# Performance work log

Measured on AMD Instinct MI355X. Metric: run time of the kernel, lower is better.

The kernel has to match this reference:

```python
import jax, jax.numpy as jnp
import numpy as np

A, C, H, W = 8, 256, 80, 108      # agents, channels, cf_h, cf_w from the module
NUM_CLASSES = 7
OUT_H, OUT_W = 256, 256


def warp_affine(feat, M):
    """Bilinear affine warp of feat [C,H,W] with sampling matrix M [2,3].
    dst(u,v) = src(M @ [u,v,1]); out-of-bounds samples are zero (kornia zero padding)."""
    c, h, w = feat.shape
    vs, us = jnp.meshgrid(jnp.arange(h, dtype=feat.dtype),
                          jnp.arange(w, dtype=feat.dtype), indexing='ij')
    sx = M[0, 0] * us + M[0, 1] * vs + M[0, 2]
    sy = M[1, 0] * us + M[1, 1] * vs + M[1, 2]
    x0 = jnp.floor(sx)
    y0 = jnp.floor(sy)
    wx = sx - x0
    wy = sy - y0
    x0i = x0.astype(jnp.int32)
    y0i = y0.astype(jnp.int32)

    def tap(yy, xx, wgt):
        valid = (yy >= 0) & (yy < h) & (xx >= 0) & (xx < w)
        yyc = jnp.clip(yy, 0, h - 1)
        xxc = jnp.clip(xx, 0, w - 1)
        return feat[:, yyc, xxc] * (wgt * valid)[None]

    return (tap(y0i, x0i, (1 - wy) * (1 - wx))
            + tap(y0i, x0i + 1, (1 - wy) * wx)
            + tap(y0i + 1, x0i, wy * (1 - wx))
            + tap(y0i + 1, x0i + 1, wy * wx))


def resize_bilinear_align_corners(img, oh, ow):
    """F.interpolate(..., mode='bilinear', align_corners=True) for img [N,C,H,W]."""
    h, w = img.shape[-2:]
    ys = jnp.linspace(0.0, h - 1.0, oh, dtype=img.dtype)
    xs = jnp.linspace(0.0, w - 1.0, ow, dtype=img.dtype)
    y0 = jnp.clip(jnp.floor(ys).astype(jnp.int32), 0, h - 2)
    x0 = jnp.clip(jnp.floor(xs).astype(jnp.int32), 0, w - 2)
    wy = (ys - y0)[None, None, :, None]
    wx = (xs - x0)[None, None, None, :]
    row = img[:, :, y0, :] * (1 - wy) + img[:, :, y0 + 1, :] * wy   # [N,C,oh,W]
    return row[:, :, :, x0] * (1 - wx) + row[:, :, :, x0 + 1] * wx  # [N,C,oh,ow]


def setup_inputs() -> dict:
    key = jax.random.key(0)
    k1, k2, k3, k4, k5, k6 = jax.random.split(key, 6)
    x = jax.random.normal(k1, (A, C, H, W), jnp.float32)
    # near-identity per-pair affine sampling matrices with small rotation/shear + translation
    rel = jnp.tile(jnp.eye(2, 3, dtype=jnp.float32), (A, A, 1, 1))
    rel = rel + 0.05 * jax.random.normal(k2, (A, A, 2, 3), jnp.float32)
    rel = rel.at[..., 2].add(10.0 * jax.random.normal(k3, (A, A, 2), jnp.float32))
    adjacency_matrix = jax.random.randint(k4, (A, A), 0, 2, dtype=jnp.int32)
    car_masks = jax.random.uniform(k5, (A, 256, 256), jnp.float32)
    w_cls = 0.02 * jax.random.normal(k6, (NUM_CLASSES, C), jnp.float32)
    b_cls = jnp.zeros((NUM_CLASSES,), jnp.float32)
    return {"x": x, "relative_tfs": rel, "adjacency_matrix": adjacency_matrix,
            "car_masks": car_masks, "w_cls": w_cls, "b_cls": b_cls}


def reference(x, relative_tfs, adjacency_matrix, car_masks, w_cls, b_cls):
    # x = x + F.interpolate(car_masks.unsqueeze(1), (cf_h, cf_w), 'bilinear')  (align_corners=False)
    cm = jax.image.resize(car_masks[:, None], (A, 1, H, W), method="bilinear")
    x = x + cm

    # aggregate_features: per ego-agent i, warp all agents' features into i's frame,
    # zero agents with adjacency[i,j]==0, and sum over j.
    warp_all = jax.vmap(warp_affine)                       # over agents j
    warped = jax.vmap(lambda Ms: warp_all(x, Ms))(relative_tfs)  # [A,A,C,H,W]
    fov = (adjacency_matrix != 0).astype(x.dtype)          # [A,A]
    aggr = jnp.einsum('ij,ijchw->ichw', fov, warped)       # masked sum over j

    def predict(f):  # mask_prediction (1x1 conv) + sigmoid
        logits = jnp.einsum('oc,achw->aohw', w_cls, f) + b_cls[None, :, None, None]
        return jax.nn.sigmoid(logits)

    solo_x = resize_bilinear_align_corners(predict(x), OUT_H, OUT_W)
    aggr_x = resize_bilinear_align_corners(predict(aggr), OUT_H, OUT_W)
    return (solo_x, aggr_x)
```

## Files before the change

### kernel.cpp

```cpp
#include <hip/hip_runtime.h>
#include <hip/hip_bf16.h>

#define A_N 8
#define C_N 256
#define H_N 80
#define W_N 108
#define P_N (H_N * W_N)
#define P4_N (P_N / 4)
#define O_N 7
#define MH 256
#define MW 256
#define OUT_HW 256
#define TPA 34
#define NCG 4

__device__ __forceinline__ float sigmoidf_(float zv) {
    return 1.0f / (1.0f + __expf(-zv));
}

__launch_bounds__(256, 2)
__global__ void k_convp(const float* __restrict__ x, const float* __restrict__ masks,
                        const float* __restrict__ w, float* __restrict__ part)
{
    __shared__ float4 s_red[O_N][NCG][64];
    __shared__ float  s_w[512];
    __shared__ float  s_cm[256];

    const int tid  = threadIdx.x;
    const int lane = tid & 63;
    const int wid  = tid >> 6;
    const int bi   = blockIdx.x;
    const int cg   = bi & 3;
    const int t2   = bi >> 2;
    const int tile = t2 % TPA;
    const int a    = t2 / TPA;

    if (tid < 64) {
        const int c = cg * 64 + tid;
        #pragma unroll
        for (int o = 0; o < 8; ++o)
            s_w[tid * 8 + o] = (o < O_N) ? w[o * C_N + c] : 0.0f;
    }

    {
        const int px = tile * 256 + tid;
        const int pc = min(px, P_N - 1);
        const int oy = pc / W_N, ox = pc - oy * W_N;
        const float ksy = 256.0f / 80.0f;
        const float ksx = 256.0f / 108.0f;
        const float rky = 0.3125f;
        const float rkx = 0.421875f;
        const float sfy = ((float)oy + 0.5f) * ksy - 0.5f;
        const float sfx = ((float)ox + 0.5f) * ksx - 0.5f;
        const int iyS = (int)ceilf(sfy - ksy);
        const int ixS = (int)ceilf(sfx - ksx);

        float wxv[5];
        float wxs = 0.0f;
        #pragma unroll
        for (int q = 0; q < 5; ++q) {
            const int ix = ixS + q;
            float wv = fmaxf(0.0f, 1.0f - fabsf(sfx - (float)ix) * rkx);
            wv = (ix >= 0 && ix < MW) ? wv : 0.0f;
            wxv[q] = wv;
            wxs += wv;
        }
        const float* mp = masks + (size_t)a * (MH * MW);
        float acm = 0.0f, wys = 0.0f;
        #pragma unroll
        for (int r = 0; r < 7; ++r) {
            const int iy = iyS + r;
            float wy = fmaxf(0.0f, 1.0f - fabsf(sfy - (float)iy) * rky);
            wy = (iy >= 0 && iy < MH) ? wy : 0.0f;
            wys += wy;
            const float* row = mp + min(max(iy, 0), MH - 1) * MW;
            float rs = 0.0f;
            #pragma unroll
            for (int q = 0; q < 5; ++q)
                rs = fmaf(wxv[q], row[min(max(ixS + q, 0), MW - 1)], rs);
            acm = fmaf(wy, rs, acm);
        }
        s_cm[tid] = acm / (wys * wxs);
    }
    __syncthreads();

    const int px4  = tile * 64 + lane;
    const int px4c = min(px4, P4_N - 1);
    const float* xp = x + ((size_t)a * C_N + cg * 64 + wid) * P_N + (size_t)px4c * 4;

#define LD(k) const float4 v##k = *reinterpret_cast<const float4*>(xp + (size_t)(4 * (k)) * P_N);
    LD(0)  LD(1)  LD(2)  LD(3)  LD(4)  LD(5)  LD(6)  LD(7)
    LD(8)  LD(9)  LD(10) LD(11) LD(12) LD(13) LD(14) LD(15)
#undef LD

    const float4 cm4 = reinterpret_cast<const float4*>(s_cm)[lane];

    float4 acc[O_N];
    #pragma unroll
    for (int o = 0; o < O_N; ++o) acc[o] = make_float4(0.f, 0.f, 0.f, 0.f);

#define FMA(k)                                                                 \
    {                                                                          \
        float4 v = v##k;                                                       \
        v.x += cm4.x; v.y += cm4.y; v.z += cm4.z; v.w += cm4.w;                \
        const float* wc = s_w + (wid + 4 * (k)) * 8;         \
        const float4 wA = *reinterpret_cast<const float4*>(wc);                \
        const float4 wB = *reinterpret_cast<const float4*>(wc + 4);            \
        acc[0].x = fmaf(wA.x, v.x, acc[0].x); acc[0].y = fmaf(wA.x, v.y, acc[0].y); \
        acc[0].z = fmaf(wA.x, v.z, acc[0].z); acc[0].w = fmaf(wA.x, v.w, acc[0].w); \
        acc[1].x = fmaf(wA.y, v.x, acc[1].x); acc[1].y = fmaf(wA.y, v.y, acc[1].y); \
        acc[1].z = fmaf(wA.y, v.z, acc[1].z); acc[1].w = fmaf(wA.y, v.w, acc[1].w); \
        acc[2].x = fmaf(wA.z, v.x, acc[2].x); acc[2].y = fmaf(wA.z, v.y, acc[2].y); \
        acc[2].z = fmaf(wA.z, v.z, acc[2].z); acc[2].w = fmaf(wA.z, v.w, acc[2].w); \
        acc[3].x = fmaf(wA.w, v.x, acc[3].x); acc[3].y = fmaf(wA.w, v.y, acc[3].y); \
        acc[3].z = fmaf(wA.w, v.z, acc[3].z); acc[3].w = fmaf(wA.w, v.w, acc[3].w); \
        acc[4].x = fmaf(wB.x, v.x, acc[4].x); acc[4].y = fmaf(wB.x, v.y, acc[4].y); \
        acc[4].z = fmaf(wB.x, v.z, acc[4].z); acc[4].w = fmaf(wB.x, v.w, acc[4].w); \
        acc[5].x = fmaf(wB.y, v.x, acc[5].x); acc[5].y = fmaf(wB.y, v.y, acc[5].y); \
        acc[5].z = fmaf(wB.y, v.z, acc[5].z); acc[5].w = fmaf(wB.y, v.w, acc[5].w); \
        acc[6].x = fmaf(wB.z, v.x, acc[6].x); acc[6].y = fmaf(wB.z, v.y, acc[6].y); \
        acc[6].z = fmaf(wB.z, v.z, acc[6].z); acc[6].w = fmaf(wB.z, v.w, acc[6].w); \
    }
    FMA(0)  FMA(1)  FMA(2)  FMA(3)  FMA(4)  FMA(5)  FMA(6)  FMA(7)
    FMA(8)  FMA(9)  FMA(10) FMA(11) FMA(12) FMA(13) FMA(14) FMA(15)
#undef FMA

    #pragma unroll
    for (int o = 0; o < O_N; ++o)
        s_red[o][wid][lane] = acc[o];
    __syncthreads();

    for (int pair = tid; pair < 64 * O_N; pair += 256) {
        const int pl = pair & 63;
        const int o  = pair >> 6;
        const int pg = tile * 64 + pl;
        if (pg >= P4_N) continue;
        const float4 s0 = s_red[o][0][pl];
        const float4 s1 = s_red[o][1][pl];
        const float4 s2 = s_red[o][2][pl];
        const float4 s3 = s_red[o][3][pl];
        float4 pv;
        pv.x = s0.x + s1.x + s2.x + s3.x;
        pv.y = s0.y + s1.y + s2.y + s3.y;
        pv.z = s0.z + s1.z + s2.z + s3.z;
        pv.w = s0.w + s1.w + s2.w + s3.w;
        reinterpret_cast<float4*>(part)[((size_t)(cg * A_N + a) * O_N + o) * P4_N + pg] = pv;
    }
}

__launch_bounds__(256)
__global__ void k_finalize(const float* __restrict__ part, const float* __restrict__ b,
                           float* __restrict__ z, float* __restrict__ ssolo)
{
    const int id = blockIdx.x * 256 + threadIdx.x;
    if (id >= A_N * O_N * P4_N) return;
    const int px4 = id % P4_N;
    const int ao  = id / P4_N;
    const int o   = ao % O_N;

    const float4* p4 = reinterpret_cast<const float4*>(part);
    float4 s = p4[((size_t)(0 * A_N * O_N) + ao) * P4_N + px4];
    #pragma unroll
    for (int g = 1; g < NCG; ++g) {
        const float4 t = p4[((size_t)(g * A_N * O_N) + ao) * P4_N + px4];
        s.x += t.x; s.y += t.y; s.z += t.z; s.w += t.w;
    }
    reinterpret_cast<float4*>(z)[(size_t)ao * P4_N + px4] = s;
    const float bo = b[o];
    float4 sv;
    sv.x = sigmoidf_(s.x + bo);
    sv.y = sigmoidf_(s.y + bo);
    sv.z = sigmoidf_(s.z + bo);
    sv.w = sigmoidf_(s.w + bo);
    reinterpret_cast<float4*>(ssolo)[(size_t)ao * P4_N + px4] = sv;
}

__launch_bounds__(64)
__global__ void k_aggr(const float* __restrict__ z, const float* __restrict__ rel,
                       const int* __restrict__ adj, const float* __restrict__ b,
                       float* __restrict__ saggr)
{
    const int i = blockIdx.x / 135;
    const int p = (blockIdx.x - i * 135) * 64 + threadIdx.x;
    const int vy = p / W_N, ux = p - vy * W_N;
    const float fu = (float)ux, fv = (float)vy;

    float acc[O_N];
    #pragma unroll
    for (int o = 0; o < O_N; ++o) acc[o] = b[o];

    for (int j = 0; j < A_N; ++j) {
        if (adj[i * A_N + j] == 0) continue;
        const float* M = rel + (i * A_N + j) * 6;
        float sx = M[0] * fu + M[1] * fv + M[2];
        float sy = M[3] * fu + M[4] * fv + M[5];
        if (!(sx > -1.0f && sx < (float)W_N && sy > -1.0f && sy < (float)H_N)) continue;
        float x0f = floorf(sx), y0f = floorf(sy);
        float wx = sx - x0f, wy = sy - y0f;
        int x0 = (int)x0f, y0 = (int)y0f;
        int x1 = x0 + 1,  y1 = y0 + 1;
        float w00 = (1.0f - wy) * (1.0f - wx), w01 = (1.0f - wy) * wx;
        float w10 = wy * (1.0f - wx),          w11 = wy * wx;
        if (x0 < 0)    { w00 = 0.0f; w10 = 0.0f; x0 = 0; }
        if (x1 >= W_N) { w01 = 0.0f; w11 = 0.0f; x1 = W_N - 1; }
        if (y0 < 0)    { w00 = 0.0f; w01 = 0.0f; y0 = 0; }
        if (y1 >= H_N) { w10 = 0.0f; w11 = 0.0f; y1 = H_N - 1; }
        const int i00 = y0 * W_N + x0, i01 = y0 * W_N + x1;
        const int i10 = y1 * W_N + x0, i11 = y1 * W_N + x1;
        const float* zj = z + j * O_N * P_N;
        #pragma unroll
        for (int o = 0; o < O_N; ++o) {
            const float* zp = zj + o * P_N;
            acc[o] += w00 * zp[i00] + w01 * zp[i01] + w10 * zp[i10] + w11 * zp[i11];
        }
    }
    const int ob = i * O_N * P_N + p;
    #pragma unroll
    for (int o = 0; o < O_N; ++o) saggr[ob + o * P_N] = sigmoidf_(acc[o]);
}

__launch_bounds__(256)
__global__ void k_upsample(const float* __restrict__ ssolo, const float* __restrict__ saggr,
                           float* __restrict__ out)
{
    const int idx = blockIdx.x * 256 + threadIdx.x;
    int k = idx;
    const int oxq = k & 63;   k >>= 6;
    const int oy  = k & 255;  k >>= 8;
    const int o   = k % O_N;  k /= O_N;
    const int a   = k & 7;    k >>= 3;
    const int t   = k;

    const float* src = (t == 0 ? ssolo : saggr) + (a * O_N + o) * P_N;
    float syf = (float)oy * (79.0f / 255.0f);
    int y0 = (int)syf; y0 = min(y0, H_N - 2);
    float wy = syf - (float)y0;
    const float* r0 = src + y0 * W_N;
    const float* r1 = r0 + W_N;

    float res[4];
    #pragma unroll
    for (int q = 0; q < 4; ++q) {
        int ox = oxq * 4 + q;
        float sxf = (float)ox * (107.0f / 255.0f);
        int x0 = (int)sxf; x0 = min(x0, W_N - 2);
        float wx = sxf - (float)x0;
        float c0 = r0[x0]     * (1.0f - wy) + r1[x0]     * wy;
        float c1 = r0[x0 + 1] * (1.0f - wy) + r1[x0 + 1] * wy;
        res[q] = c0 * (1.0f - wx) + c1 * wx;
    }
    *reinterpret_cast<float4*>(out + (size_t)idx * 4) =
        make_float4(res[0], res[1], res[2], res[3]);
}

extern "C" void kernel_launch(void* const* d_in, const int* in_sizes, int n_in,
                              void* d_out, int out_size, void* d_ws, size_t ws_size,
                              hipStream_t stream)
{
    (void)in_sizes; (void)n_in; (void)out_size; (void)ws_size;
    const float* x    = (const float*)d_in[0];
    const float* rel  = (const float*)d_in[1];
    const int*   adj  = (const int*)d_in[2];
    const float* cmsk = (const float*)d_in[3];
    const float* wcls = (const float*)d_in[4];
    const float* bcls = (const float*)d_in[5];
    float* out = (float*)d_out;

    float* ws    = (float*)d_ws;
    float* part  = ws;
    float* z     = part  + NCG * A_N * O_N * P_N;
    float* ssolo = z     + A_N * O_N * P_N;
    float* saggr = ssolo + A_N * O_N * P_N;

    k_convp   <<<A_N * TPA * NCG, 256, 0, stream>>>(x, cmsk, wcls, part);
    k_finalize<<<(A_N * O_N * P4_N + 255) / 256, 256, 0, stream>>>(part, bcls, z, ssolo);
    k_aggr    <<<1080, 64, 0, stream>>>(z, rel, adj, bcls, saggr);
    k_upsample<<<7168, 256, 0, stream>>>(ssolo, saggr, out);
}
```

Measured before the change: 43.36 us.

## Hoist car-mask term out of conv via weight row-sums and split channel work

The 1x1 conv no longer adds the resized car mask to every channel. It computes the per-output sum of weights once and adds sum_w*cm a single time, in the cg==0 block only. Each thread now owns 4 pixels over 32 channels with pipelined loads, replacing the cross-wave LDS reduction. The number of channel groups doubles, so the partial buffer and finalize reads grow. The aggr kernel also splits the j-loop across two waves with a shared-memory combine to raise parallelism.

```diff
diff --git a/kernel.cpp b/kernel.cpp
--- a/kernel.cpp
+++ b/kernel.cpp
@@ -11,99 +11,109 @@
 #define MH 256
 #define MW 256
 #define OUT_HW 256
-#define TPA 34
-#define NCG 4
+#define TPA 17
+#define NCG 8
+#define GCH 32
 
 __device__ __forceinline__ float sigmoidf_(float zv) {
     return 1.0f / (1.0f + __expf(-zv));
 }
 
-__launch_bounds__(256, 2)
+__launch_bounds__(128, 4)
 __global__ void k_convp(const float* __restrict__ x, const float* __restrict__ masks,
                         const float* __restrict__ w, float* __restrict__ part)
 {
-    __shared__ float4 s_red[O_N][NCG][64];
-    __shared__ float  s_w[512];
-    __shared__ float  s_cm[256];
+    __shared__ float s_w[GCH * 8];
+    __shared__ float s_cm[512];
+    __shared__ float s_wpart[112];
+    __shared__ float s_wsum[O_N];
 
     const int tid  = threadIdx.x;
-    const int lane = tid & 63;
-    const int wid  = tid >> 6;
     const int bi   = blockIdx.x;
-    const int cg   = bi & 3;
-    const int t2   = bi >> 2;
+    const int cg   = bi & 7;
+    const int t2   = bi >> 3;
     const int tile = t2 % TPA;
     const int a    = t2 / TPA;
 
-    if (tid < 64) {
-        const int c = cg * 64 + tid;
-        #pragma unroll
-        for (int o = 0; o < 8; ++o)
-            s_w[tid * 8 + o] = (o < O_N) ? w[o * C_N + c] : 0.0f;
-    }
-
-    {
-        const int px = tile * 256 + tid;
-        const int pc = min(px, P_N - 1);
-        const int oy = pc / W_N, ox = pc - oy * W_N;
-        const float ksy = 256.0f / 80.0f;
-        const float ksx = 256.0f / 108.0f;
-        const float rky = 0.3125f;
-        const float rkx = 0.421875f;
-        const float sfy = ((float)oy + 0.5f) * ksy - 0.5f;
-        const float sfx = ((float)ox + 0.5f) * ksx - 0.5f;
-        const int iyS = (int)ceilf(sfy - ksy);
-        const int ixS = (int)ceilf(sfx - ksx);
-
-        float wxv[5];
-        float wxs = 0.0f;
-        #pragma unroll
-        for (int q = 0; q < 5; ++q) {
-            const int ix = ixS + q;
-            float wv = fmaxf(0.0f, 1.0f - fabsf(sfx - (float)ix) * rkx);
-            wv = (ix >= 0 && ix < MW) ? wv : 0.0f;
-            wxv[q] = wv;
-            wxs += wv;
+    #pragma unroll
+    for (int r = 0; r < 2; ++r) {
+        const int e = r * 128 + tid;
+        const int cl = e >> 3, o = e & 7;
+        s_w[e] = (o < O_N) ? w[o * C_N + cg * GCH + cl] : 0.0f;
+    }
+
+    if (cg == 0) {
+        if (tid < 112) {
+            const int o = tid >> 4, seg = tid & 15;
+            const float4* wr = reinterpret_cast<const float4*>(w + o * C_N + seg * 16);
+            float s = 0.0f;
+            #pragma unroll
+            for (int q = 0; q < 4; ++q) { float4 v = wr[q]; s += v.x + v.y + v.z + v.w; }
+            s_wpart[tid] = s;
         }
-        const float* mp = masks + (size_t)a * (MH * MW);
-        float acm = 0.0f, wys = 0.0f;
-        #pragma unroll
-        for (int r = 0; r < 7; ++r) {
-            const int iy = iyS + r;
-            float wy = fmaxf(0.0f, 1.0f - fabsf(sfy - (float)iy) * rky);
-            wy = (iy >= 0 && iy < MH) ? wy : 0.0f;
-            wys += wy;
-            const float* row = mp + min(max(iy, 0), MH - 1) * MW;
-            float rs = 0.0f;
+        #pragma unroll
+        for (int q4 = 0; q4 < 4; ++q4) {
+            const int pi = tid * 4 + q4;
+            const int px = min(tile * 512 + pi, P_N - 1);
+            const int oy = px / W_N, ox = px - oy * W_N;
+            const float ksy = 256.0f / 80.0f;
+            const float ksx = 256.0f / 108.0f;
+            const float rky = 0.3125f;
+            const float rkx = 0.421875f;
+            const float sfy = ((float)oy + 0.5f) * ksy - 0.5f;
+            const float sfx = ((float)ox + 0.5f) * ksx - 0.5f;
+            const int iyS = (int)ceilf(sfy - ksy);
+            const int ixS = (int)ceilf(sfx - ksx);
+            float wxv[5];
+            float wxs = 0.0f;
             #pragma unroll
-            for (int q = 0; q < 5; ++q)
-                rs = fmaf(wxv[q], row[min(max(ixS + q, 0), MW - 1)], rs);
-            acm = fmaf(wy, rs, acm);
+            for (int q = 0; q < 5; ++q) {
+                const int ix = ixS + q;
+                float wv = fmaxf(0.0f, 1.0f - fabsf(sfx - (float)ix) * rkx);
+                wv = (ix >= 0 && ix < MW) ? wv : 0.0f;
+                wxv[q] = wv;
+                wxs += wv;
+            }
+            const float* mp = masks + (size_t)a * (MH * MW);
+            float acm = 0.0f, wys = 0.0f;
+            #pragma unroll
+            for (int r = 0; r < 7; ++r) {
+                const int iy = iyS + r;
+                float wy = fmaxf(0.0f, 1.0f - fabsf(sfy - (float)iy) * rky);
+                wy = (iy >= 0 && iy < MH) ? wy : 0.0f;
+                wys += wy;
+                const float* row = mp + min(max(iy, 0), MH - 1) * MW;
+                float rs = 0.0f;
+                #pragma unroll
+                for (int q = 0; q < 5; ++q)
+                    rs = fmaf(wxv[q], row[min(max(ixS + q, 0), MW - 1)], rs);
+                acm = fmaf(wy, rs, acm);
+            }
+            s_cm[pi] = acm / (wys * wxs);
         }
-        s_cm[tid] = acm / (wys * wxs);
     }
     __syncthreads();
-
-    const int px4  = tile * 64 + lane;
+    if (cg == 0 && tid < O_N) {
+        float s = 0.0f;
+        #pragma unroll
+        for (int g = 0; g < 16; ++g) s += s_wpart[tid * 16 + g];
+        s_wsum[tid] = s;
+    }
+    __syncthreads();
+
+    const int px4  = tile * 128 + tid;
     const int px4c = min(px4, P4_N - 1);
-    const float* xp = x + ((size_t)a * C_N + cg * 64 + wid) * P_N + (size_t)px4c * 4;
-
-#define LD(k) const float4 v##k = *reinterpret_cast<const float4*>(xp + (size_t)(4 * (k)) * P_N);
-    LD(0)  LD(1)  LD(2)  LD(3)  LD(4)  LD(5)  LD(6)  LD(7)
-    LD(8)  LD(9)  LD(10) LD(11) LD(12) LD(13) LD(14) LD(15)
-#undef LD
-
-    const float4 cm4 = reinterpret_cast<const float4*>(s_cm)[lane];
+    const float* xp = x + ((size_t)(a * C_N + cg * GCH)) * P_N + (size_t)px4c * 4;
 
     float4 acc[O_N];
     #pragma unroll
     for (int o = 0; o < O_N; ++o) acc[o] = make_float4(0.f, 0.f, 0.f, 0.f);
 
+#define LD(k) const float4 v##k = *reinterpret_cast<const float4*>(xp + (size_t)(k) * P_N);
 #define FMA(k)                                                                 \
     {                                                                          \
-        float4 v = v##k;                                                       \
-        v.x += cm4.x; v.y += cm4.y; v.z += cm4.z; v.w += cm4.w;                \
-        const float* wc = s_w + (wid + 4 * (k)) * 8;         \
+        const float4 v = v##k;                                                 \
+        const float* wc = s_w + (k) * 8;                     \
         const float4 wA = *reinterpret_cast<const float4*>(wc);                \
         const float4 wB = *reinterpret_cast<const float4*>(wc + 4);            \
         acc[0].x = fmaf(wA.x, v.x, acc[0].x); acc[0].y = fmaf(wA.x, v.y, acc[0].y); \
@@ -121,30 +131,45 @@
         acc[6].x = fmaf(wB.z, v.x, acc[6].x); acc[6].y = fmaf(wB.z, v.y, acc[6].y); \
         acc[6].z = fmaf(wB.z, v.z, acc[6].z); acc[6].w = fmaf(wB.z, v.w, acc[6].w); \
     }
-    FMA(0)  FMA(1)  FMA(2)  FMA(3)  FMA(4)  FMA(5)  FMA(6)  FMA(7)
-    FMA(8)  FMA(9)  FMA(10) FMA(11) FMA(12) FMA(13) FMA(14) FMA(15)
+    LD(0)  LD(1)  LD(2)  LD(3)  LD(4)  LD(5)  LD(6)  LD(7)
+    LD(8)  LD(9)  LD(10) LD(11) LD(12) LD(13) LD(14) LD(15)
+    FMA(0)  LD(16)
+    FMA(1)  LD(17)
+    FMA(2)  LD(18)
+    FMA(3)  LD(19)
+    FMA(4)  LD(20)
+    FMA(5)  LD(21)
+    FMA(6)  LD(22)
+    FMA(7)  LD(23)
+    FMA(8)  LD(24)
+    FMA(9)  LD(25)
+    FMA(10) LD(26)
+    FMA(11) LD(27)
+    FMA(12) LD(28)
+    FMA(13) LD(29)
+    FMA(14) LD(30)
+    FMA(15) LD(31)
+    FMA(16) FMA(17) FMA(18) FMA(19) FMA(20) FMA(21) FMA(22) FMA(23)
+    FMA(24) FMA(25) FMA(26) FMA(27) FMA(28) FMA(29) FMA(30) FMA(31)
+#undef LD
 #undef FMA
 
-    #pragma unroll
-    for (int o = 0; o < O_N; ++o)
-        s_red[o][wid][lane] = acc[o];
-    __syncthreads();
-
-    for (int pair = tid; pair < 64 * O_N; pair += 256) {
-        const int pl = pair & 63;
-        const int o  = pair >> 6;
-        const int pg = tile * 64 + pl;
-        if (pg >= P4_N) continue;
-        const float4 s0 = s_red[o][0][pl];
-        const float4 s1 = s_red[o][1][pl];
-        const float4 s2 = s_red[o][2][pl];
-        const float4 s3 = s_red[o][3][pl];
-        float4 pv;
-        pv.x = s0.x + s1.x + s2.x + s3.x;
-        pv.y = s0.y + s1.y + s2.y + s3.y;
-        pv.z = s0.z + s1.z + s2.z + s3.z;
-        pv.w = s0.w + s1.w + s2.w + s3.w;
-        reinterpret_cast<float4*>(part)[((size_t)(cg * A_N + a) * O_N + o) * P4_N + pg] = pv;
+    if (cg == 0) {
+        const float4 cm4 = reinterpret_cast<const float4*>(s_cm)[tid];
+        #pragma unroll
+        for (int o = 0; o < O_N; ++o) {
+            const float ws = s_wsum[o];
+            acc[o].x = fmaf(ws, cm4.x, acc[o].x);
+            acc[o].y = fmaf(ws, cm4.y, acc[o].y);
+            acc[o].z = fmaf(ws, cm4.z, acc[o].z);
+            acc[o].w = fmaf(ws, cm4.w, acc[o].w);
+        }
+    }
+
+    if (px4 < P4_N) {
+        #pragma unroll
+        for (int o = 0; o < O_N; ++o)
+            reinterpret_cast<float4*>(part)[((size_t)(cg * A_N + a) * O_N + o) * P4_N + px4] = acc[o];
     }
 }
 
@@ -159,7 +184,7 @@
     const int o   = ao % O_N;
 
     const float4* p4 = reinterpret_cast<const float4*>(part);
-    float4 s = p4[((size_t)(0 * A_N * O_N) + ao) * P4_N + px4];
+    float4 s = p4[(size_t)ao * P4_N + px4];
     #pragma unroll
     for (int g = 1; g < NCG; ++g) {
         const float4 t = p4[((size_t)(g * A_N * O_N) + ao) * P4_N + px4];
@@ -175,21 +200,25 @@
     reinterpret_cast<float4*>(ssolo)[(size_t)ao * P4_N + px4] = sv;
 }
 
-__launch_bounds__(64)
+__launch_bounds__(128)
 __global__ void k_aggr(const float* __restrict__ z, const float* __restrict__ rel,
                        const int* __restrict__ adj, const float* __restrict__ b,
                        float* __restrict__ saggr)
 {
+    __shared__ float s_p[O_N][64];
+    const int tid  = threadIdx.x;
+    const int lane = tid & 63;
+    const int jb   = (tid >> 6) * 4;
     const int i = blockIdx.x / 135;
-    const int p = (blockIdx.x - i * 135) * 64 + threadIdx.x;
+    const int p = (blockIdx.x - i * 135) * 64 + lane;
     const int vy = p / W_N, ux = p - vy * W_N;
     const float fu = (float)ux, fv = (float)vy;
 
     float acc[O_N];
     #pragma unroll
-    for (int o = 0; o < O_N; ++o) acc[o] = b[o];
-
-    for (int j = 0; j < A_N; ++j) {
+    for (int o = 0; o < O_N; ++o) acc[o] = (jb == 0) ? b[o] : 0.0f;
+
+    for (int j = jb; j < jb + 4; ++j) {
         if (adj[i * A_N + j] == 0) continue;
         const float* M = rel + (i * A_N + j) * 6;
         float sx = M[0] * fu + M[1] * fv + M[2];
@@ -214,9 +243,17 @@
             acc[o] += w00 * zp[i00] + w01 * zp[i01] + w10 * zp[i10] + w11 * zp[i11];
         }
     }
-    const int ob = i * O_N * P_N + p;
-    #pragma unroll
-    for (int o = 0; o < O_N; ++o) saggr[ob + o * P_N] = sigmoidf_(acc[o]);
+    if (tid >= 64) {
+        #pragma unroll
+        for (int o = 0; o < O_N; ++o) s_p[o][lane] = acc[o];
+    }
+    __syncthreads();
+    if (tid < 64) {
+        const int ob = i * O_N * P_N + p;
+        #pragma unroll
+        for (int o = 0; o < O_N; ++o)
+            saggr[ob + o * P_N] = sigmoidf_(acc[o] + s_p[o][lane]);
+    }
 }
 
 __launch_bounds__(256)
@@ -272,8 +309,8 @@
     float* ssolo = z     + A_N * O_N * P_N;
     float* saggr = ssolo + A_N * O_N * P_N;
 
-    k_convp   <<<A_N * TPA * NCG, 256, 0, stream>>>(x, cmsk, wcls, part);
+    k_convp   <<<A_N * TPA * NCG, 128, 0, stream>>>(x, cmsk, wcls, part);
     k_finalize<<<(A_N * O_N * P4_N + 255) / 256, 256, 0, stream>>>(part, bcls, z, ssolo);
-    k_aggr    <<<1080, 64, 0, stream>>>(z, rel, adj, bcls, saggr);
+    k_aggr    <<<1080, 128, 0, stream>>>(z, rel, adj, bcls, saggr);
     k_upsample<<<7168, 256, 0, stream>>>(ssolo, saggr, out);
 }
```

After: 56.62 us. +30.6%, slower.
